# Kernel tuning notes

Measured on AMD Instinct MI355X. Metric: run time of the kernel, lower is better.

## Reference

```python
import jax, jax.numpy as jnp
import numpy as np

N_NODES = 50000
N_EDGES = 800000
D_IN = 64
D_OUT = 64


def setup_inputs() -> dict:
    key = jax.random.key(0)
    k_x, k_s, k_d, k_w, k_b = jax.random.split(key, 5)
    x = jax.random.normal(k_x, (N_NODES, D_IN), dtype=jnp.float32)
    src = jax.random.randint(k_s, (N_EDGES,), 0, N_NODES, dtype=jnp.int64)
    dst = jax.random.randint(k_d, (N_EDGES,), 0, N_NODES, dtype=jnp.int64)
    W = jax.random.normal(k_w, (D_OUT, D_IN), dtype=jnp.float32) / np.sqrt(D_IN)
    b = jax.random.normal(k_b, (D_OUT,), dtype=jnp.float32) * 0.01
    return {"x": x, "src": src, "dst": dst, "W": W, "b": b}


def reference(x, src, dst, W, b):
    # update_all(copy_u('h','m'), mean('m','h')): for each node v,
    # h[v] = mean over incoming edges (u->v) of x[u]; 0 if in-degree == 0.
    msgs = x[src]  # [E, D_IN] gather (irregular access)
    summed = jax.ops.segment_sum(msgs, dst, num_segments=N_NODES)  # [N, D_IN]
    deg = jax.ops.segment_sum(jnp.ones((src.shape[0],), dtype=x.dtype), dst,
                              num_segments=N_NODES)  # [N]
    h = summed / jnp.maximum(deg, 1.0)[:, None]  # zero-degree nodes stay 0
    # dense linear: h @ W.T + b
    return jnp.einsum("nd,od->no", h, W) + b
```

## Files before the change

### kernel.cpp

```cpp
#include <hip/hip_runtime.h>

#define N_NODES 50000
#define N_EDGES 800000
#define SLOTS 64
#define ZROW 50000
#define XROWS 50048
#define NBUCKET 196
#define BNODES 256
#define CAP 8192
#define NCHUNK 256
#define CE 3125
#define NCVT 400000
#define NTILES 3125

typedef short bf16x8 __attribute__((ext_vector_type(8)));
typedef float f32x4 __attribute__((ext_vector_type(4)));

__device__ __forceinline__ unsigned short f2bf(float f) {
    unsigned int u = __float_as_uint(f);
    unsigned int r = (u + 0x7fffu + ((u >> 16) & 1u)) >> 16;
    return (unsigned short)r;
}
__device__ __forceinline__ float bflo(unsigned int u) { return __uint_as_float(u << 16); }
__device__ __forceinline__ float bfhi(unsigned int u) { return __uint_as_float(u & 0xffff0000u); }

__global__ __launch_bounds__(256)
void gcn_bin(const int* __restrict__ src, const int* __restrict__ dst,
             const float4* __restrict__ x4,
             unsigned int* __restrict__ pbuf, int* __restrict__ gcur,
             uint4* __restrict__ xb) {
    __shared__ int hist[NBUCKET];
    __shared__ int gbase[NBUCKET];
    int tid = threadIdx.x;
    int chunk = blockIdx.x;
    for (int i = tid; i < NBUCKET; i += 256) hist[i] = 0;
    __syncthreads();

    int lo = chunk * CE;
    unsigned int pairr[13];
    unsigned int kp[13];
#pragma unroll
    for (int j = 0; j < 13; ++j) {
        int off = tid + j * 256;
        kp[j] = 0xFFFFFFFFu;
        if (off < CE) {
            int d = dst[lo + off];
            int s = src[lo + off];
            int key = d >> 8;
            int pos = atomicAdd(&hist[key], 1);
            pairr[j] = ((unsigned int)d << 16) | (unsigned int)s;
            kp[j] = ((unsigned int)key << 16) | (unsigned int)pos;
        }
    }
    __syncthreads();
    if (tid < NBUCKET) gbase[tid] = atomicAdd(&gcur[tid], hist[tid]);
    __syncthreads();
#pragma unroll
    for (int j = 0; j < 13; ++j) {
        if (kp[j] != 0xFFFFFFFFu) {
            int key = (int)(kp[j] >> 16);
            int idx = gbase[key] + (int)(kp[j] & 0xFFFFu);
            if (idx < CAP) pbuf[key * CAP + idx] = pairr[j];
        }
    }

    int gi = chunk * 256 + tid;
    if (gi < 8) xb[(size_t)ZROW * 8 + gi] = make_uint4(0u, 0u, 0u, 0u);

    for (int i = gi; i < NCVT; i += NCHUNK * 256) {
        float4 a = x4[i * 2];
        float4 c = x4[i * 2 + 1];
        uint4 o;
        o.x = (unsigned)f2bf(a.x) | ((unsigned)f2bf(a.y) << 16);
        o.y = (unsigned)f2bf(a.z) | ((unsigned)f2bf(a.w) << 16);
        o.z = (unsigned)f2bf(c.x) | ((unsigned)f2bf(c.y) << 16);
        o.w = (unsigned)f2bf(c.z) | ((unsigned)f2bf(c.w) << 16);
        xb[i] = o;
    }
}

__global__ __launch_bounds__(256)
void gcn_build(const unsigned int* __restrict__ pbuf,
               const int* __restrict__ gcur,
               unsigned short* __restrict__ ell,
               unsigned short* __restrict__ deg) {
    __shared__ int cnt[BNODES];
    __shared__ unsigned short lell[BNODES * SLOTS];
    int key = blockIdx.x;
    int tid = threadIdx.x;
    cnt[tid] = 0;
    uint4* lf = (uint4*)lell;
    const uint4 pad = make_uint4(0xC350C350u, 0xC350C350u, 0xC350C350u, 0xC350C350u);
    for (int i = tid; i < BNODES * SLOTS / 8; i += 256) lf[i] = pad;
    __syncthreads();

    int m = min(gcur[key], CAP);
    int base = key * CAP;
    for (int i = tid; i < m; i += 256) {
        unsigned int u = pbuf[base + i];
        int dl = (int)(u >> 16) & 255;
        int pos = atomicAdd(&cnt[dl], 1);
        if (pos < SLOTS) lell[dl * SLOTS + pos] = (unsigned short)(u & 0xFFFFu);
    }
    __syncthreads();

    uint4* eg = (uint4*)(ell + (size_t)key * BNODES * SLOTS);
    const uint4* ls = (const uint4*)lell;
    for (int i = tid; i < BNODES * SLOTS / 8; i += 256) eg[i] = ls[i];
    deg[key * BNODES + tid] = (unsigned short)min(cnt[tid], SLOTS);
}

__global__ __launch_bounds__(256)
void gcn_gather(const uint4* __restrict__ xb4,
                const unsigned short* __restrict__ deg,
                const unsigned short* __restrict__ ell,
                uint4* __restrict__ hb4) {
    int lane = threadIdx.x & 63;
    int node = (blockIdx.x << 2) | (threadIdx.x >> 6);
    if (node >= N_NODES) return;

    int c = (int)deg[node];
    int cr = (c + 7) & ~7;
    int myid = (int)ell[node * SLOTS + lane];

    int g = lane >> 3;
    int col = lane & 7;

    float a0 = 0.f, a1 = 0.f, a2 = 0.f, a3 = 0.f;
    float a4 = 0.f, a5 = 0.f, a6 = 0.f, a7 = 0.f;
#pragma unroll 2
    for (int k = 0; k < cr; k += 8) {
        int sid = __shfl(myid, k + g, 64);
        uint4 v = xb4[sid * 8 + col];
        a0 += bflo(v.x); a1 += bfhi(v.x);
        a2 += bflo(v.y); a3 += bfhi(v.y);
        a4 += bflo(v.z); a5 += bfhi(v.z);
        a6 += bflo(v.w); a7 += bfhi(v.w);
    }
#pragma unroll
    for (int off = 8; off < 64; off <<= 1) {
        a0 += __shfl_xor(a0, off, 64); a1 += __shfl_xor(a1, off, 64);
        a2 += __shfl_xor(a2, off, 64); a3 += __shfl_xor(a3, off, 64);
        a4 += __shfl_xor(a4, off, 64); a5 += __shfl_xor(a5, off, 64);
        a6 += __shfl_xor(a6, off, 64); a7 += __shfl_xor(a7, off, 64);
    }

    if (g == 0) {
        float inv = c > 0 ? 1.0f / (float)c : 0.0f;
        uint4 o;
        o.x = (unsigned)f2bf(a0 * inv) | ((unsigned)f2bf(a1 * inv) << 16);
        o.y = (unsigned)f2bf(a2 * inv) | ((unsigned)f2bf(a3 * inv) << 16);
        o.z = (unsigned)f2bf(a4 * inv) | ((unsigned)f2bf(a5 * inv) << 16);
        o.w = (unsigned)f2bf(a6 * inv) | ((unsigned)f2bf(a7 * inv) << 16);
        hb4[node * 8 + col] = o;
    }
}

__global__ __launch_bounds__(256)
void gcn_gemm(const unsigned int* __restrict__ hbu,
              const float* __restrict__ W,
              const float* __restrict__ b,
              float* __restrict__ out) {
    int lane = threadIdx.x & 63;
    int tile = (blockIdx.x << 2) | (threadIdx.x >> 6);
    if (tile >= NTILES) return;

    int row = lane & 15;
    int quad = lane >> 4;
    int base = tile * 16;

    bf16x8 bfrag[4][2];
#pragma unroll
    for (int nt = 0; nt < 4; ++nt) {
#pragma unroll
        for (int kc = 0; kc < 2; ++kc) {
            const float* wp = &W[(nt * 16 + row) * 64 + kc * 32 + quad * 8];
            float4 w0 = *(const float4*)wp;
            float4 w1 = *(const float4*)(wp + 4);
            bf16x8 f;
            f[0] = (short)f2bf(w0.x); f[1] = (short)f2bf(w0.y);
            f[2] = (short)f2bf(w0.z); f[3] = (short)f2bf(w0.w);
            f[4] = (short)f2bf(w1.x); f[5] = (short)f2bf(w1.y);
            f[6] = (short)f2bf(w1.z); f[7] = (short)f2bf(w1.w);
            bfrag[nt][kc] = f;
        }
    }

    bf16x8 afrag[2];
#pragma unroll
    for (int kc = 0; kc < 2; ++kc) {
        uint4 av = *(const uint4*)&hbu[(base + row) * 32 + kc * 16 + quad * 4];
        afrag[kc] = *(const bf16x8*)&av;
    }

    f32x4 d[4] = {{0.f, 0.f, 0.f, 0.f}, {0.f, 0.f, 0.f, 0.f},
                  {0.f, 0.f, 0.f, 0.f}, {0.f, 0.f, 0.f, 0.f}};
#pragma unroll
    for (int nt = 0; nt < 4; ++nt) {
#pragma unroll
        for (int kc = 0; kc < 2; ++kc) {
            d[nt] = __builtin_amdgcn_mfma_f32_16x16x32_bf16(
                afrag[kc], bfrag[nt][kc], d[nt], 0, 0, 0);
        }
    }

#pragma unroll
    for (int nt = 0; nt < 4; ++nt) {
        float bias = b[nt * 16 + row];
#pragma unroll
        for (int r = 0; r < 4; ++r) {
            out[(base + quad * 4 + r) * 64 + nt * 16 + row] = d[nt][r] + bias;
        }
    }
}

extern "C" void kernel_launch(void* const* d_in, const int* in_sizes, int n_in,
                              void* d_out, int out_size, void* d_ws, size_t ws_size,
                              hipStream_t stream) {
    const float* x   = (const float*)d_in[0];
    const int*   src = (const int*)d_in[1];
    const int*   dst = (const int*)d_in[2];
    const float* W   = (const float*)d_in[3];
    const float* b   = (const float*)d_in[4];
    float* out = (float*)d_out;

    unsigned int* pbuf = (unsigned int*)d_ws;
    int* gcur = (int*)(pbuf + (size_t)NBUCKET * CAP);
    unsigned short* ell = (unsigned short*)(gcur + 256);
    unsigned short* deg = ell + (size_t)NBUCKET * BNODES * SLOTS;
    unsigned short* xb  = deg + NBUCKET * BNODES;
    unsigned int*   hb  = (unsigned int*)(xb + (size_t)XROWS * 64);

    hipMemsetAsync(gcur, 0, 256 * sizeof(int), stream);
    gcn_bin<<<NCHUNK, 256, 0, stream>>>(src, dst, (const float4*)x,
                                        pbuf, gcur, (uint4*)xb);
    gcn_build<<<NBUCKET, 256, 0, stream>>>(pbuf, gcur, ell, deg);
    gcn_gather<<<(N_NODES + 3) / 4, 256, 0, stream>>>(
        (const uint4*)xb, deg, ell, (uint4*)hb);
    gcn_gemm<<<(NTILES + 3) / 4, 256, 0, stream>>>(hb, W, b, out);
}
```

Before: 67.32 us.

## Fuse gather and GEMM kernels via LDS tile; per-wave histograms in binning

Merges the neighbor-mean gather and the bf16 MFMA GEMM into one kernel. Each block aggregates 16 nodes into an LDS tile, then one wave runs the 16x64x64 MFMA from LDS, so the intermediate h no longer makes a global round trip and one launch is removed. In the binning kernel, the shared histogram is split into per-wave copies with prefix offsets to reduce LDS atomic contention. In exchange, only one of four waves does the GEMM, and each wave now processes four nodes serially, which lowers gather parallelism per wave.

```diff
diff --git a/kernel.cpp b/kernel.cpp
--- a/kernel.cpp
+++ b/kernel.cpp
@@ -29,11 +29,13 @@
              const float4* __restrict__ x4,
              unsigned int* __restrict__ pbuf, int* __restrict__ gcur,
              uint4* __restrict__ xb) {
-    __shared__ int hist[NBUCKET];
+    __shared__ int hist[4][NBUCKET];
+    __shared__ int wpre[4][NBUCKET];
     __shared__ int gbase[NBUCKET];
     int tid = threadIdx.x;
+    int wid = tid >> 6;
     int chunk = blockIdx.x;
-    for (int i = tid; i < NBUCKET; i += 256) hist[i] = 0;
+    for (int i = tid; i < 4 * NBUCKET; i += 256) ((int*)hist)[i] = 0;
     __syncthreads();
 
     int lo = chunk * CE;
@@ -47,19 +49,27 @@
             int d = dst[lo + off];
             int s = src[lo + off];
             int key = d >> 8;
-            int pos = atomicAdd(&hist[key], 1);
+            int pos = atomicAdd(&hist[wid][key], 1);
             pairr[j] = ((unsigned int)d << 16) | (unsigned int)s;
             kp[j] = ((unsigned int)key << 16) | (unsigned int)pos;
         }
     }
     __syncthreads();
-    if (tid < NBUCKET) gbase[tid] = atomicAdd(&gcur[tid], hist[tid]);
+    if (tid < NBUCKET) {
+        int c0 = hist[0][tid], c1 = hist[1][tid];
+        int c2 = hist[2][tid], c3 = hist[3][tid];
+        wpre[0][tid] = 0;
+        wpre[1][tid] = c0;
+        wpre[2][tid] = c0 + c1;
+        wpre[3][tid] = c0 + c1 + c2;
+        gbase[tid] = atomicAdd(&gcur[tid], c0 + c1 + c2 + c3);
+    }
     __syncthreads();
 #pragma unroll
     for (int j = 0; j < 13; ++j) {
         if (kp[j] != 0xFFFFFFFFu) {
             int key = (int)(kp[j] >> 16);
-            int idx = gbase[key] + (int)(kp[j] & 0xFFFFu);
+            int idx = gbase[key] + wpre[wid][key] + (int)(kp[j] & 0xFFFFu);
             if (idx < CAP) pbuf[key * CAP + idx] = pairr[j];
         }
     }
@@ -111,59 +121,56 @@
 }
 
 __global__ __launch_bounds__(256)
-void gcn_gather(const uint4* __restrict__ xb4,
-                const unsigned short* __restrict__ deg,
-                const unsigned short* __restrict__ ell,
-                uint4* __restrict__ hb4) {
-    int lane = threadIdx.x & 63;
-    int node = (blockIdx.x << 2) | (threadIdx.x >> 6);
-    if (node >= N_NODES) return;
-
-    int c = (int)deg[node];
-    int cr = (c + 7) & ~7;
-    int myid = (int)ell[node * SLOTS + lane];
-
+void gcn_gather_gemm(const uint4* __restrict__ xb4,
+                     const unsigned short* __restrict__ deg,
+                     const unsigned short* __restrict__ ell,
+                     const float* __restrict__ W,
+                     const float* __restrict__ b,
+                     float* __restrict__ out) {
+    __shared__ uint4 lh[16][9];
+    int tid = threadIdx.x;
+    int lane = tid & 63;
+    int w = tid >> 6;
+    int tile = blockIdx.x;
     int g = lane >> 3;
     int col = lane & 7;
 
-    float a0 = 0.f, a1 = 0.f, a2 = 0.f, a3 = 0.f;
-    float a4 = 0.f, a5 = 0.f, a6 = 0.f, a7 = 0.f;
-#pragma unroll 2
-    for (int k = 0; k < cr; k += 8) {
-        int sid = __shfl(myid, k + g, 64);
-        uint4 v = xb4[sid * 8 + col];
-        a0 += bflo(v.x); a1 += bfhi(v.x);
-        a2 += bflo(v.y); a3 += bfhi(v.y);
-        a4 += bflo(v.z); a5 += bfhi(v.z);
-        a6 += bflo(v.w); a7 += bfhi(v.w);
-    }
-#pragma unroll
-    for (int off = 8; off < 64; off <<= 1) {
-        a0 += __shfl_xor(a0, off, 64); a1 += __shfl_xor(a1, off, 64);
-        a2 += __shfl_xor(a2, off, 64); a3 += __shfl_xor(a3, off, 64);
-        a4 += __shfl_xor(a4, off, 64); a5 += __shfl_xor(a5, off, 64);
-        a6 += __shfl_xor(a6, off, 64); a7 += __shfl_xor(a7, off, 64);
-    }
-
-    if (g == 0) {
-        float inv = c > 0 ? 1.0f / (float)c : 0.0f;
-        uint4 o;
-        o.x = (unsigned)f2bf(a0 * inv) | ((unsigned)f2bf(a1 * inv) << 16);
-        o.y = (unsigned)f2bf(a2 * inv) | ((unsigned)f2bf(a3 * inv) << 16);
-        o.z = (unsigned)f2bf(a4 * inv) | ((unsigned)f2bf(a5 * inv) << 16);
-        o.w = (unsigned)f2bf(a6 * inv) | ((unsigned)f2bf(a7 * inv) << 16);
-        hb4[node * 8 + col] = o;
-    }
-}
-
-__global__ __launch_bounds__(256)
-void gcn_gemm(const unsigned int* __restrict__ hbu,
-              const float* __restrict__ W,
-              const float* __restrict__ b,
-              float* __restrict__ out) {
-    int lane = threadIdx.x & 63;
-    int tile = (blockIdx.x << 2) | (threadIdx.x >> 6);
-    if (tile >= NTILES) return;
+#pragma unroll
+    for (int i = 0; i < 4; ++i) {
+        int node = tile * 16 + w * 4 + i;
+        int c = (int)deg[node];
+        int cr = (c + 7) & ~7;
+        int myid = (int)ell[node * SLOTS + lane];
+
+        float a0 = 0.f, a1 = 0.f, a2 = 0.f, a3 = 0.f;
+        float a4 = 0.f, a5 = 0.f, a6 = 0.f, a7 = 0.f;
+        for (int k = 0; k < cr; k += 8) {
+            int sid = __shfl(myid, k + g, 64);
+            uint4 v = xb4[sid * 8 + col];
+            a0 += bflo(v.x); a1 += bfhi(v.x);
+            a2 += bflo(v.y); a3 += bfhi(v.y);
+            a4 += bflo(v.z); a5 += bfhi(v.z);
+            a6 += bflo(v.w); a7 += bfhi(v.w);
+        }
+#pragma unroll
+        for (int off = 8; off < 64; off <<= 1) {
+            a0 += __shfl_xor(a0, off, 64); a1 += __shfl_xor(a1, off, 64);
+            a2 += __shfl_xor(a2, off, 64); a3 += __shfl_xor(a3, off, 64);
+            a4 += __shfl_xor(a4, off, 64); a5 += __shfl_xor(a5, off, 64);
+            a6 += __shfl_xor(a6, off, 64); a7 += __shfl_xor(a7, off, 64);
+        }
+        if (g == 0) {
+            float inv = c > 0 ? 1.0f / (float)c : 0.0f;
+            uint4 o;
+            o.x = (unsigned)f2bf(a0 * inv) | ((unsigned)f2bf(a1 * inv) << 16);
+            o.y = (unsigned)f2bf(a2 * inv) | ((unsigned)f2bf(a3 * inv) << 16);
+            o.z = (unsigned)f2bf(a4 * inv) | ((unsigned)f2bf(a5 * inv) << 16);
+            o.w = (unsigned)f2bf(a6 * inv) | ((unsigned)f2bf(a7 * inv) << 16);
+            lh[w * 4 + i][col] = o;
+        }
+    }
+    __syncthreads();
+    if (w != 0) return;
 
     int row = lane & 15;
     int quad = lane >> 4;
@@ -189,7 +196,7 @@
     bf16x8 afrag[2];
 #pragma unroll
     for (int kc = 0; kc < 2; ++kc) {
-        uint4 av = *(const uint4*)&hbu[(base + row) * 32 + kc * 16 + quad * 4];
+        uint4 av = lh[row][kc * 4 + quad];
         afrag[kc] = *(const bf16x8*)&av;
     }
 
@@ -229,13 +236,11 @@
     unsigned short* ell = (unsigned short*)(gcur + 256);
     unsigned short* deg = ell + (size_t)NBUCKET * BNODES * SLOTS;
     unsigned short* xb  = deg + NBUCKET * BNODES;
-    unsigned int*   hb  = (unsigned int*)(xb + (size_t)XROWS * 64);
 
     hipMemsetAsync(gcur, 0, 256 * sizeof(int), stream);
     gcn_bin<<<NCHUNK, 256, 0, stream>>>(src, dst, (const float4*)x,
                                         pbuf, gcur, (uint4*)xb);
     gcn_build<<<NBUCKET, 256, 0, stream>>>(pbuf, gcur, ell, deg);
-    gcn_gather<<<(N_NODES + 3) / 4, 256, 0, stream>>>(
-        (const uint4*)xb, deg, ell, (uint4*)hb);
-    gcn_gemm<<<(NTILES + 3) / 4, 256, 0, stream>>>(hb, W, b, out);
-}
+    gcn_gather_gemm<<<NTILES, 256, 0, stream>>>(
+        (const uint4*)xb, deg, ell, W, b, out);
+}
```

Result: no change. 66.58 us (-1.1%).
